# Optimization experiments

Hardware: AMD Instinct MI355X
Metric: run time of the kernel (lower is better)

Reference implementation:

```python
import jax, jax.numpy as jnp
import numpy as np

N_NODES = 20000   # N
N_EDGES = 320000  # E (avg degree 16)
T_STEPS = 16      # T
IN_FEATS = 1      # F
HG = 64           # hidden_g
HT = 128          # hidden_t
LN_EPS = 1e-5


def _layer_norm(x, g, b):
    mu = jnp.mean(x, axis=-1, keepdims=True)
    var = jnp.mean((x - mu) ** 2, axis=-1, keepdims=True)
    return (x - mu) * jax.lax.rsqrt(var + LN_EPS) * g + b


def setup_inputs() -> dict:
    key = jax.random.key(0)
    k = jax.random.split(key, 16)
    r = lambda i, shape, s: jax.random.normal(k[i], shape, jnp.float32) * s
    return dict(
        x_seq=jax.random.normal(k[0], (1, T_STEPS, N_NODES, IN_FEATS), jnp.float32),
        edge_index=jax.random.randint(k[1], (2, N_EDGES), 0, N_NODES, dtype=jnp.int32),
        # SAGEConv layer 0: lin_l (aggregated neighbors, has bias) + lin_r (root)
        W_l0=r(2, (IN_FEATS, HG), 0.5), W_r0=r(3, (IN_FEATS, HG), 0.5), b0=jnp.zeros((HG,), jnp.float32),
        ln0_g=jnp.ones((HG,), jnp.float32), ln0_b=jnp.zeros((HG,), jnp.float32),
        # SAGEConv layer 1
        W_l1=r(4, (HG, HG), 0.1), W_r1=r(5, (HG, HG), 0.1), b1=jnp.zeros((HG,), jnp.float32),
        ln1_g=jnp.ones((HG,), jnp.float32), ln1_b=jnp.zeros((HG,), jnp.float32),
        # GRU (torch layout: gates r,z,n stacked along first dim)
        gru_Wih=r(6, (3 * HT, HG), 0.05), gru_Whh=r(7, (3 * HT, HT), 0.05),
        gru_bih=jnp.zeros((3 * HT,), jnp.float32), gru_bhh=jnp.zeros((3 * HT,), jnp.float32),
        # head
        head_W=r(8, (HT, 1), 0.05), head_b=jnp.zeros((1,), jnp.float32),
    )


def reference(x_seq, edge_index, W_l0, W_r0, b0, ln0_g, ln0_b,
              W_l1, W_r1, b1, ln1_g, ln1_b,
              gru_Wih, gru_Whh, gru_bih, gru_bhh, head_W, head_b):
    src, dst = edge_index[0], edge_index[1]
    # in-degree for mean aggregation (clamped to 1, like PyG mean aggr on isolated nodes)
    deg = jnp.clip(jax.ops.segment_sum(jnp.ones((N_EDGES,), jnp.float32), dst,
                                       num_segments=N_NODES), 1.0)[:, None]

    def sage(x, Wl, Wr, b):
        # mean over incoming neighbors, then lin_l(aggr) + lin_r(root)
        agg = jax.ops.segment_sum(x[src], dst, num_segments=N_NODES) / deg
        return agg @ Wl + x @ Wr + b

    def stack(xt):  # xt: (N, F) -> (N, HG); dropout is identity in eval mode
        h = jax.nn.relu(_layer_norm(sage(xt, W_l0, W_r0, b0), ln0_g, ln0_b))
        h = jax.nn.relu(_layer_norm(sage(h, W_l1, W_r1, b1), ln1_g, ln1_b))
        return h

    X = x_seq[0]  # (T, N, F), B == 1
    # scan over timesteps (matches the per-t Python loop, bounds peak memory)
    _, H = jax.lax.scan(lambda c, xt: (c, stack(xt)), None, X)  # H: (T, N, HG)

    def gru_step(h, xt):  # torch GRU cell; batch = N nodes
        gi = xt @ gru_Wih.T + gru_bih
        gh = h @ gru_Whh.T + gru_bhh
        ir, iz, inn = jnp.split(gi, 3, axis=-1)
        hr, hz, hn = jnp.split(gh, 3, axis=-1)
        r = jax.nn.sigmoid(ir + hr)
        z = jax.nn.sigmoid(iz + hz)
        n = jnp.tanh(inn + r * hn)
        return (1.0 - z) * n + z * h, None

    h0 = jnp.zeros((N_NODES, HT), x_seq.dtype)
    hT, _ = jax.lax.scan(gru_step, h0, H)
    y = (hT @ head_W + head_b)[:, 0]  # (N,)
    return y
```

## Files before the change

### kernel.cpp

```cpp
#include <hip/hip_runtime.h>
#include <math.h>

#define NN 20000
#define NE 320000
#define TS 16
#define HG 64
#define HTT 128
#define NG 384
#define LN_EPS 1e-5f

typedef __attribute__((ext_vector_type(8))) _Float16 f16x8;
typedef __attribute__((ext_vector_type(4))) _Float16 f16x4;
typedef __attribute__((ext_vector_type(2))) _Float16 f16x2;
typedef __attribute__((ext_vector_type(4))) float f32x4;

__device__ __forceinline__ float wave_sum64(float v) {
  #pragma unroll
  for (int off = 32; off > 0; off >>= 1) v += __shfl_xor(v, off, 64);
  return v;
}
__device__ __forceinline__ float quad_sum16(float v) {
  #pragma unroll
  for (int off = 1; off < 16; off <<= 1) v += __shfl_xor(v, off, 64);
  return v;
}
__device__ __forceinline__ float fast_sigmoid(float x) {
  return __builtin_amdgcn_rcpf(1.f + __expf(-x));
}
__device__ __forceinline__ float fast_tanh(float x) {
  float e = __expf(-2.f * fabsf(x));
  float th = (1.f - e) * __builtin_amdgcn_rcpf(1.f + e);
  return copysignf(th, x);
}

__global__ __launch_bounds__(256) void k_setup(
    const float* __restrict__ x_seq, float* __restrict__ xT,
    const float* __restrict__ Wih, _Float16* __restrict__ WihF,
    const float* __restrict__ Whh, _Float16* __restrict__ WhhF,
    const float* __restrict__ Wl1, const float* __restrict__ Wr1,
    _Float16* __restrict__ Wchi, _Float16* __restrict__ Wclo,
    const float* __restrict__ Wl0, const float* __restrict__ Wr0,
    const float* __restrict__ b0, const float* __restrict__ g0,
    const float* __restrict__ be0, float* __restrict__ P,
    int* __restrict__ cnt) {
  int gid = blockIdx.x * 256 + threadIdx.x;
  int stride = gridDim.x * 256;
  for (int i = gid; i < NN * TS; i += stride) {
    int t = i / NN, n = i - t * NN;
    xT[n * 16 + t] = x_seq[i];
  }
  for (int i = gid; i < NG * HG; i += stride) WihF[i] = (_Float16)Wih[i];
  for (int i = gid; i < NG * HTT; i += stride) WhhF[i] = (_Float16)Whh[i];
  for (int i = gid; i < HG * 128; i += stride) {
    int n = i >> 7, k = i & 127;
    float x = (k < HG) ? Wl1[k * HG + n] : Wr1[(k - HG) * HG + n];
    _Float16 h = (_Float16)x;
    Wchi[i] = h;
    Wclo[i] = (_Float16)(x - (float)h);
  }
  for (int i = gid; i < NN; i += stride) cnt[i] = 0;
  if (blockIdx.x == 0 && threadIdx.x < 64) {
    int f = threadIdx.x;
    float u = Wl0[f], v = Wr0[f], c = b0[f], g = g0[f];
    float um = wave_sum64(u) * (1.f / 64.f);
    float vm = wave_sum64(v) * (1.f / 64.f);
    float cm = wave_sum64(c) * (1.f / 64.f);
    float uc = u - um, vc = v - vm, cc = c - cm;
    float muu = wave_sum64(uc * uc) * (1.f / 64.f);
    float mvv = wave_sum64(vc * vc) * (1.f / 64.f);
    float mcc = wave_sum64(cc * cc) * (1.f / 64.f);
    float muv = wave_sum64(uc * vc) * (1.f / 64.f);
    float muc = wave_sum64(uc * cc) * (1.f / 64.f);
    float mvc = wave_sum64(vc * cc) * (1.f / 64.f);
    P[f] = uc * g; P[64 + f] = vc * g; P[128 + f] = cc * g; P[192 + f] = be0[f];
    if (f == 0) {
      P[256] = muu; P[257] = mvv; P[258] = mcc;
      P[259] = muv; P[260] = muc; P[261] = mvc;
    }
  }
}

__global__ void k_hist(const int* __restrict__ dst, int* cnt) {
  int e = blockIdx.x * blockDim.x + threadIdx.x;
  if (e < NE) atomicAdd(&cnt[dst[e]], 1);
}

__global__ void k_scan(int* cnt, int* row_ptr, float* deg_inv) {
  __shared__ int s[1024];
  const int PER = 20;
  int tid = threadIdx.x;
  int base = tid * PER;
  int vloc[PER], dloc[PER];
  int sum = 0;
  #pragma unroll
  for (int j = 0; j < PER; j++) {
    int n = base + j;
    int d = (n < NN) ? cnt[n] : 0;
    vloc[j] = sum;
    dloc[j] = d;
    sum += d;
  }
  s[tid] = sum;
  __syncthreads();
  for (int off = 1; off < 1024; off <<= 1) {
    int t = (tid >= off) ? s[tid - off] : 0;
    __syncthreads();
    s[tid] += t;
    __syncthreads();
  }
  int excl = s[tid] - sum;
  #pragma unroll
  for (int j = 0; j < PER; j++) {
    int n = base + j;
    if (n < NN) {
      int rp = excl + vloc[j];
      row_ptr[n] = rp;
      cnt[n] = rp;
      int d = dloc[j];
      deg_inv[n] = 1.0f / (float)((d > 1) ? d : 1);
    }
  }
  if (tid == 1023) row_ptr[NN] = s[1023];
}

__global__ void k_fill(const int* __restrict__ src, const int* __restrict__ dst,
                       int* cursor, int* col) {
  int e = blockIdx.x * blockDim.x + threadIdx.x;
  if (e < NE) {
    int p = atomicAdd(&cursor[dst[e]], 1);
    col[p] = src[e];
  }
}

__global__ __launch_bounds__(256) void k_h0_fused(
    const float* __restrict__ xT,
    const int* __restrict__ row_ptr, const int* __restrict__ col,
    const float* __restrict__ deg_inv,
    const float* __restrict__ P,
    _Float16* __restrict__ h0r,
    _Float16* __restrict__ code2) {
  int lane = threadIdx.x & 63;
  int n = blockIdx.x * 4 + (threadIdx.x >> 6);
  int grp = lane >> 4, tl = lane & 15;
  int beg = row_ptr[n];
  int deg = row_ptr[n + 1] - beg;
  float s0 = 0.f, s1 = 0.f;
  int iters = (deg + 7) >> 3;
  for (int it = 0; it < iters; it++) {
    int e0 = it * 8 + grp, e1 = it * 8 + 4 + grp;
    bool v0 = e0 < deg, v1 = e1 < deg;
    int i0 = v0 ? e0 : 0, i1 = v1 ? e1 : 0;
    int c0 = col[beg + i0];
    int c1 = col[beg + i1];
    float x0 = xT[c0 * 16 + tl];
    float x1 = xT[c1 * 16 + tl];
    s0 += v0 ? x0 : 0.f;
    s1 += v1 ? x1 : 0.f;
  }
  float s = s0 + s1;
  s += __shfl_xor(s, 16, 64);
  s += __shfl_xor(s, 32, 64);
  float aggv = s * deg_inv[n];
  float xv = xT[n * 16 + tl];
  float muu = P[256], mvv = P[257], mcc = P[258];
  float muv = P[259], muc = P[260], mvc = P[261];
  if (lane < 16) {
    float a = aggv, x = xv;
    float var = a * a * muu + x * x * mvv + mcc
              + 2.f * (a * x * muv + a * muc + x * mvc);
    float rstd = rsqrtf(var + LN_EPS);
    _Float16 Ah = (_Float16)(a * rstd);
    _Float16 Xh = (_Float16)(x * rstd);
    _Float16 Ch = (_Float16)rstd;
    f16x8 cw = {Ah, Ah, Xh, Xh, Ch, Ch, (_Float16)0.f, (_Float16)0.f};
    *(f16x8*)&code2[(size_t)n * 128 + (lane & 7) * 16 + (lane >> 3) * 8] = cw;
  }
  #pragma unroll
  for (int half = 0; half < 2; half++) {
    int c = lane + half * 64;
    int t = c >> 3, f8 = (c & 7) * 8;
    float a = __shfl(aggv, t, 64);
    float x = __shfl(xv, t, 64);
    float var = a * a * muu + x * x * mvv + mcc
              + 2.f * (a * x * muv + a * muc + x * mvc);
    float rstd = rsqrtf(var + LN_EPS);
    f16x8 o;
    #pragma unroll
    for (int j = 0; j < 8; j++) {
      int f = f8 + j;
      float d = a * P[f] + x * P[64 + f] + P[128 + f];
      o[j] = (_Float16)fmaxf(d * rstd + P[192 + f], 0.f);
    }
    *(f16x8*)&h0r[(size_t)n * 1024 + c * 8] = o;
  }
}

__global__ __launch_bounds__(256) void k_gather(
    const int* __restrict__ row_ptr, const int* __restrict__ col,
    const _Float16* __restrict__ code2,
    const float* __restrict__ P,
    _Float16* __restrict__ agg) {
  int lane = threadIdx.x & 63;
  int n = blockIdx.x * 4 + (threadIdx.x >> 6);
  const f16x2 h2z = {(_Float16)0.f, (_Float16)0.f};
  const f16x2 h2o = {(_Float16)1.f, (_Float16)1.f};
  int f1 = (lane & 7) * 8;
  int tmod = lane >> 3;
  f16x2 Pu2[4], Pv2[4], Pc2[4], Pb2[4];
  #pragma unroll
  for (int j = 0; j < 4; j++) {
    Pu2[j] = (f16x2){(_Float16)P[f1 + 2*j],       (_Float16)P[f1 + 2*j + 1]};
    Pv2[j] = (f16x2){(_Float16)P[64 + f1 + 2*j],  (_Float16)P[64 + f1 + 2*j + 1]};
    Pc2[j] = (f16x2){(_Float16)P[128 + f1 + 2*j], (_Float16)P[128 + f1 + 2*j + 1]};
    Pb2[j] = (f16x2){(_Float16)P[192 + f1 + 2*j], (_Float16)P[192 + f1 + 2*j + 1]};
  }
  int beg = row_ptr[n];
  int deg = row_ptr[n + 1] - beg;
  int cvAll = (lane < deg) ? col[beg + lane] : 0;

  f16x2 aE1[4], aO1[4], aE2[4], aO2[4];
  #pragma unroll
  for (int j = 0; j < 4; j++) { aE1[j] = h2z; aO1[j] = h2z; aE2[j] = h2z; aO2[j] = h2z; }

#define ACC_SET(c, mk, FULL, ACC)                                          \
  { f16x2 _A = __builtin_shufflevector(c, c, 0, 1);                        \
    f16x2 _X = __builtin_shufflevector(c, c, 2, 3);                        \
    f16x2 _C = __builtin_shufflevector(c, c, 4, 5);                        \
    _Pragma("unroll")                                                      \
    for (int j = 0; j < 4; j++) {                                          \
      f16x2 d = __builtin_elementwise_fma(_A, Pu2[j],                      \
                 __builtin_elementwise_fma(_X, Pv2[j],                     \
                  __builtin_elementwise_fma(_C, Pc2[j], Pb2[j])));         \
      d = __builtin_elementwise_max(d, h2z);                               \
      ACC[j] = (FULL) ? (ACC[j] + d)                                       \
                      : __builtin_elementwise_fma(d, mk, ACC[j]);          \
    } }

#define LOADBLK(CA, CB, EB)                                                \
  { _Pragma("unroll")                                                      \
    for (int e = 0; e < 4; e++) {                                          \
      int c = __builtin_amdgcn_readlane(cvAll, (EB) + e);                  \
      const _Float16* cp = code2 + (size_t)c * 128 + tmod * 16;            \
      CA[e] = *(const f16x8*)cp;                                           \
      CB[e] = *(const f16x8*)(cp + 8);                                     \
    } }

#define ACCBLK(CA, CB, EB)                                                 \
  { if ((EB) + 4 <= deg) {                                                 \
      _Pragma("unroll")                                                    \
      for (int e = 0; e < 4; e++) {                                        \
        if (e & 1) { ACC_SET(CA[e], h2o, true, aO1) ACC_SET(CB[e], h2o, true, aO2) } \
        else       { ACC_SET(CA[e], h2o, true, aE1) ACC_SET(CB[e], h2o, true, aE2) } \
      }                                                                    \
    } else {                                                               \
      _Pragma("unroll")                                                    \
      for (int e = 0; e < 4; e++) {                                        \
        f16x2 mk = (((EB) + e) < deg) ? h2o : h2z;                         \
        if (e & 1) { ACC_SET(CA[e], mk, false, aO1) ACC_SET(CB[e], mk, false, aO2) } \
        else       { ACC_SET(CA[e], mk, false, aE1) ACC_SET(CB[e], mk, false, aE2) } \
      }                                                                    \
    } }

  int nb4 = (deg + 3) >> 2;
  if (nb4 > 16) nb4 = 16;
  {
    f16x8 cA[4], cB[4], nA[4], nB[4];
    if (nb4 > 0) LOADBLK(cA, cB, 0)
    int b = 0;
    while (b < nb4) {
      if (b + 1 < nb4) LOADBLK(nA, nB, (b + 1) << 2)
      ACCBLK(cA, cB, b << 2)
      b++;
      if (b >= nb4) break;
      if (b + 1 < nb4) LOADBLK(cA, cB, (b + 1) << 2)
      ACCBLK(nA, nB, b << 2)
      b++;
    }
  }
  for (int e = 64; e < deg; e++) {
    int c = col[beg + e];
    const _Float16* cp = code2 + (size_t)c * 128 + tmod * 16;
    f16x8 ca = *(const f16x8*)cp;
    f16x8 cb = *(const f16x8*)(cp + 8);
    ACC_SET(ca, h2o, true, aE1) ACC_SET(cb, h2o, true, aE2)
  }
#undef ACCBLK
#undef LOADBLK
#undef ACC_SET

  float dif = 1.0f / (float)((deg > 1) ? deg : 1);
  _Float16 dih = (_Float16)dif;
  f16x2 di2 = {dih, dih};
  union { f16x8 v; f16x2 h[4]; } u0, u1;
  #pragma unroll
  for (int j = 0; j < 4; j++) {
    u0.h[j] = (aE1[j] + aO1[j]) * di2;
    u1.h[j] = (aE2[j] + aO2[j]) * di2;
  }
  *(f16x8*)&agg[(size_t)n * 1024 + lane * 8] = u0.v;
  *(f16x8*)&agg[(size_t)n * 1024 + 512 + lane * 8] = u1.v;
}

__global__ __launch_bounds__(256) void k_gemm(
    const _Float16* __restrict__ h0r,
    const _Float16* __restrict__ agg,
    const _Float16* __restrict__ Wchi, const _Float16* __restrict__ Wclo,
    const float* __restrict__ b1, const float* __restrict__ g1, const float* __restrict__ be1,
    _Float16* __restrict__ Ht_all) {
  int tid = threadIdx.x;
  int lane = tid & 63, wave = tid >> 6;
  int col16 = lane & 15, quad = lane >> 4;
  int m0 = blockIdx.x * 16;

  float bias[4], gg[4], bb[4];
  #pragma unroll
  for (int nt = 0; nt < 4; nt++) {
    int nf = nt * 16 + col16;
    bias[nt] = b1[nf]; gg[nt] = g1[nf]; bb[nt] = be1[nf];
  }
  size_t rowbase = (size_t)(m0 + col16) * 1024;

  for (int ts = 0; ts < 4; ts++) {
    int t = wave * 4 + ts;
    f32x4 acc[4];
    #pragma unroll
    for (int nt = 0; nt < 4; nt++) acc[nt] = (f32x4){0.f, 0.f, 0.f, 0.f};

    f16x8 aa[2], ar[2];
    #pragma unroll
    for (int kk = 0; kk < 2; kk++) {
      aa[kk] = *(const f16x8*)&agg[rowbase + t * 64 + kk * 32 + quad * 8];
      ar[kk] = *(const f16x8*)&h0r[rowbase + t * 64 + kk * 32 + quad * 8];
    }
    #pragma unroll
    for (int kk = 0; kk < 2; kk++) {
      #pragma unroll
      for (int nt = 0; nt < 4; nt++) {
        int nf = nt * 16 + col16;
        f16x8 bh = *(const f16x8*)&Wchi[nf * 128 + kk * 32 + quad * 8];
        f16x8 bl = *(const f16x8*)&Wclo[nf * 128 + kk * 32 + quad * 8];
        acc[nt] = __builtin_amdgcn_mfma_f32_16x16x32_f16(aa[kk], bh, acc[nt], 0, 0, 0);
        acc[nt] = __builtin_amdgcn_mfma_f32_16x16x32_f16(aa[kk], bl, acc[nt], 0, 0, 0);
      }
    }
    #pragma unroll
    for (int kk = 0; kk < 2; kk++) {
      #pragma unroll
      for (int nt = 0; nt < 4; nt++) {
        int nf = nt * 16 + col16;
        f16x8 bh = *(const f16x8*)&Wchi[nf * 128 + 64 + kk * 32 + quad * 8];
        f16x8 bl = *(const f16x8*)&Wclo[nf * 128 + 64 + kk * 32 + quad * 8];
        acc[nt] = __builtin_amdgcn_mfma_f32_16x16x32_f16(ar[kk], bh, acc[nt], 0, 0, 0);
        acc[nt] = __builtin_amdgcn_mfma_f32_16x16x32_f16(ar[kk], bl, acc[nt], 0, 0, 0);
      }
    }

    #pragma unroll
    for (int r = 0; r < 4; r++) {
      float v[4];
      #pragma unroll
      for (int nt = 0; nt < 4; nt++) v[nt] = acc[nt][r] + bias[nt];
      float s = (v[0] + v[1]) + (v[2] + v[3]);
      float mu = quad_sum16(s) * (1.f / 64.f);
      float sq = 0.f;
      #pragma unroll
      for (int nt = 0; nt < 4; nt++) { v[nt] -= mu; sq += v[nt] * v[nt]; }
      float var = quad_sum16(sq) * (1.f / 64.f);
      float rstd = rsqrtf(var + LN_EPS);
      int m = m0 + quad * 4 + r;
      size_t base = ((size_t)t * NN + m) * HG;
      #pragma unroll
      for (int nt = 0; nt < 4; nt++) {
        float o = fmaxf(v[nt] * rstd * gg[nt] + bb[nt], 0.f);
        Ht_all[base + nt * 16 + col16] = (_Float16)o;
      }
    }
  }
}

__global__ __launch_bounds__(256, 2) void k_gru_all(
    const _Float16* __restrict__ Ht_all,
    const _Float16* __restrict__ WihF,
    const _Float16* __restrict__ WhhF,
    const float* __restrict__ bih, const float* __restrict__ bhh,
    const float* __restrict__ headW, const float* __restrict__ headb,
    float* __restrict__ out) {
  __shared__ _Float16 WihL[NG * 64];
  __shared__ _Float16 hL[2][32 * 128];
  __shared__ float yL[4][32];

  int tid = threadIdx.x;
  int lane = tid & 63, wave = tid >> 6;
  int col16 = lane & 15, quad = lane >> 4;
  int m0 = blockIdx.x * 32;
  int gb = 2 * wave;

  for (int i = tid; i < NG * 8; i += 256) {
    int g = i >> 3, k8 = i & 7;
    *(f16x8*)&WihL[g * 64 + ((k8 + g) & 7) * 8] = *(const f16x8*)&WihF[g * 64 + k8 * 8];
  }
  for (int i = tid; i < 2 * 32 * 128; i += 256) hL[0][i] = (_Float16)0.f;

  int gts[6];
  #pragma unroll
  for (int t6 = 0; t6 < 6; t6++)
    gts[t6] = (t6 < 2) ? (gb + t6) : (t6 < 4) ? (8 + gb + t6 - 2) : (16 + gb + t6 - 4);

  f16x8 wgh[4][6];
  #pragma unroll
  for (int kk = 0; kk < 4; kk++)
    #pragma unroll
    for (int t6 = 0; t6 < 6; t6++)
      wgh[kk][t6] = *(const f16x8*)&WhhF[(size_t)(gts[t6] * 16 + col16) * HTT + kk * 32 + quad * 8];

  float bR[2], bZ[2], bNi[2], bNh[2], hw[2];
  int waddr[2][4][2];
  #pragma unroll
  for (int js = 0; js < 2; js++) {
    int j = (gb + js) * 16 + col16;
    bR[js]  = bih[j] + bhh[j];
    bZ[js]  = bih[HTT + j] + bhh[HTT + j];
    bNi[js] = bih[2 * HTT + j];
    bNh[js] = bhh[2 * HTT + j];
    hw[js]  = headW[j];
    #pragma unroll
    for (int mt = 0; mt < 2; mt++)
      #pragma unroll
      for (int r = 0; r < 4; r++) {
        int row = mt * 16 + quad * 4 + r;
        waddr[mt][r][js] = row * 128 + (((j >> 3) + row) & 15) * 8 + (j & 7);
      }
  }
  float hreg[2][4][2];
  #pragma unroll
  for (int mt = 0; mt < 2; mt++)
    #pragma unroll
    for (int r = 0; r < 4; r++) { hreg[mt][r][0] = 0.f; hreg[mt][r][1] = 0.f; }

  size_t aoff[2][2];
  #pragma unroll
  for (int kk = 0; kk < 2; kk++)
    #pragma unroll
    for (int mt = 0; mt < 2; mt++)
      aoff[kk][mt] = (size_t)(m0 + mt * 16 + col16) * HG + kk * 32 + quad * 8;

  f16x8 gah[2][2];
  #pragma unroll
  for (int kk = 0; kk < 2; kk++)
    #pragma unroll
    for (int mt = 0; mt < 2; mt++)
      gah[kk][mt] = *(const f16x8*)&Ht_all[aoff[kk][mt]];

  __syncthreads();

  for (int t = 0; t < TS; t++) {
    const _Float16* hcur = hL[t & 1];
    _Float16* hnxt = hL[(t + 1) & 1];

    f32x4 acc[8][2];
    #pragma unroll
    for (int a = 0; a < 8; a++) {
      acc[a][0] = (f32x4){0.f, 0.f, 0.f, 0.f};
      acc[a][1] = (f32x4){0.f, 0.f, 0.f, 0.f};
    }

    #pragma unroll
    for (int kk = 0; kk < 2; kk++) {
      #pragma unroll
      for (int t6 = 0; t6 < 6; t6++) {
        int g = gts[t6] * 16 + col16;
        int k8 = kk * 4 + quad;
        f16x8 b = *(const f16x8*)&WihL[g * 64 + ((k8 + g) & 7) * 8];
        #pragma unroll
        for (int mt = 0; mt < 2; mt++)
          acc[t6][mt] = __builtin_amdgcn_mfma_f32_16x16x32_f16(gah[kk][mt], b, acc[t6][mt], 0, 0, 0);
      }
    }

    if (t + 1 < TS) {
      const _Float16* AHn = Ht_all + (size_t)(t + 1) * NN * HG;
      #pragma unroll
      for (int kk = 0; kk < 2; kk++)
        #pragma unroll
        for (int mt = 0; mt < 2; mt++)
          gah[kk][mt] = *(const f16x8*)&AHn[aoff[kk][mt]];
    }

    #pragma unroll
    for (int kk = 0; kk < 4; kk++) {
      f16x8 ah[2];
      #pragma unroll
      for (int mt = 0; mt < 2; mt++) {
        int row = mt * 16 + col16;
        int k8 = kk * 4 + quad;
        ah[mt] = *(const f16x8*)&hcur[row * 128 + ((k8 + row) & 15) * 8];
      }
      #pragma unroll
      for (int t6 = 0; t6 < 6; t6++) {
        int ai = (t6 < 4) ? t6 : t6 + 2;
        #pragma unroll
        for (int mt = 0; mt < 2; mt++)
          acc[ai][mt] = __builtin_amdgcn_mfma_f32_16x16x32_f16(ah[mt], wgh[kk][t6], acc[ai][mt], 0, 0, 0);
      }
    }

    #pragma unroll
    for (int mt = 0; mt < 2; mt++) {
      #pragma unroll
      for (int r = 0; r < 4; r++) {
        #pragma unroll
        for (int js = 0; js < 2; js++) {
          float R  = acc[0 + js][mt][r] + bR[js];
          float Z  = acc[2 + js][mt][r] + bZ[js];
          float Ni = acc[4 + js][mt][r] + bNi[js];
          float Nh = acc[6 + js][mt][r] + bNh[js];
          float rg = fast_sigmoid(R);
          float zg = fast_sigmoid(Z);
          float nn = fast_tanh(Ni + rg * Nh);
          float hn = nn + zg * (hreg[mt][r][js] - nn);
          hreg[mt][r][js] = hn;
          hnxt[waddr[mt][r][js]] = (_Float16)hn;
        }
      }
    }
    __syncthreads();
  }

  #pragma unroll
  for (int mt = 0; mt < 2; mt++) {
    #pragma unroll
    for (int r = 0; r < 4; r++) {
      float py = hreg[mt][r][0] * hw[0] + hreg[mt][r][1] * hw[1];
      py = quad_sum16(py);
      if (col16 == 0) yL[wave][mt * 16 + quad * 4 + r] = py;
    }
  }
  __syncthreads();
  if (tid < 32)
    out[m0 + tid] = yL[0][tid] + yL[1][tid] + yL[2][tid] + yL[3][tid] + headb[0];
}

extern "C" void kernel_launch(void* const* d_in, const int* in_sizes, int n_in,
                              void* d_out, int out_size, void* d_ws, size_t ws_size,
                              hipStream_t stream) {
  const float* x_seq = (const float*)d_in[0];
  const int*   edge  = (const int*)d_in[1];
  const float* Wl0   = (const float*)d_in[2];
  const float* Wr0   = (const float*)d_in[3];
  const float* b0    = (const float*)d_in[4];
  const float* g0    = (const float*)d_in[5];
  const float* be0   = (const float*)d_in[6];
  const float* Wl1   = (const float*)d_in[7];
  const float* Wr1   = (const float*)d_in[8];
  const float* b1    = (const float*)d_in[9];
  const float* g1    = (const float*)d_in[10];
  const float* be1   = (const float*)d_in[11];
  const float* Wih   = (const float*)d_in[12];
  const float* Whh   = (const float*)d_in[13];
  const float* bih   = (const float*)d_in[14];
  const float* bhh   = (const float*)d_in[15];
  const float* headW = (const float*)d_in[16];
  const float* headb = (const float*)d_in[17];
  float* out = (float*)d_out;

  const int* srcp = edge;
  const int* dstp = edge + NE;

  char* ws = (char*)d_ws;
  size_t off = 0;
  auto alloc = [&](size_t bytes) -> void* {
    void* p = ws + off;
    off += (bytes + 255) & ~(size_t)255;
    return p;
  };
  int*   cnt     = (int*)alloc(NN * 4);
  int*   row_ptr = (int*)alloc((NN + 1) * 4);
  int*   col     = (int*)alloc(NE * 4);
  float* deg_inv = (float*)alloc(NN * 4);
  float* xT      = (float*)alloc((size_t)NN * TS * 4);
  float* P       = (float*)alloc(512 * 4);
  _Float16* h0r  = (_Float16*)alloc((size_t)NN * 1024 * 2);
  _Float16* code2= (_Float16*)alloc((size_t)NN * 128 * 2);
  _Float16* agg  = (_Float16*)alloc((size_t)NN * 1024 * 2);
  _Float16* Ht_all = (_Float16*)alloc((size_t)TS * NN * HG * 2);
  _Float16* WihF = (_Float16*)alloc((size_t)NG * HG * 2);
  _Float16* WhhF = (_Float16*)alloc((size_t)NG * HTT * 2);
  _Float16* Wchi = (_Float16*)alloc((size_t)HG * 128 * 2);
  _Float16* Wclo = (_Float16*)alloc((size_t)HG * 128 * 2);
  (void)ws_size; (void)in_sizes; (void)n_in; (void)out_size;

  k_setup<<<1250, 256, 0, stream>>>(x_seq, xT, Wih, WihF, Whh, WhhF,
                                    Wl1, Wr1, Wchi, Wclo,
                                    Wl0, Wr0, b0, g0, be0, P, cnt);
  k_hist<<<(NE + 255) / 256, 256, 0, stream>>>(dstp, cnt);
  k_scan<<<1, 1024, 0, stream>>>(cnt, row_ptr, deg_inv);
  k_fill<<<(NE + 255) / 256, 256, 0, stream>>>(srcp, dstp, cnt, col);
  k_h0_fused<<<NN / 4, 256, 0, stream>>>(xT, row_ptr, col, deg_inv, P, h0r, code2);
  k_gather<<<NN / 4, 256, 0, stream>>>(row_ptr, col, code2, P, agg);
  k_gemm<<<NN / 16, 256, 0, stream>>>(h0r, agg, Wchi, Wclo, b1, g1, be1, Ht_all);
  k_gru_all<<<NN / 32, 256, 0, stream>>>(Ht_all, WihF, WhhF, bih, bhh,
                                         headW, headb, out);
}
```

Baseline: 384.6 us.

## Recompute layer-0 activations in GEMM from compact code; fold histogram into setup

Stops materializing the full layer-0 activation tensor h0r (N×16×64 fp16). The GEMM kernel now rebuilds each root row from the per-node, per-timestep code (a·rstd, x·rstd, rstd) and the precomputed LN parameters using packed fp16 FMAs. This removes a large global write and read. The edge in-degree histogram also moves into the setup kernel, and a memset zeroes the counts, which drops one launch. The cost is extra ALU work in the GEMM, and the affine and ReLU now run in fp16 instead of fp32, which may add rounding error.

```diff
diff --git a/kernel.cpp b/kernel.cpp
--- a/kernel.cpp
+++ b/kernel.cpp
@@ -42,13 +42,14 @@
     const float* __restrict__ Wl0, const float* __restrict__ Wr0,
     const float* __restrict__ b0, const float* __restrict__ g0,
     const float* __restrict__ be0, float* __restrict__ P,
-    int* __restrict__ cnt) {
+    const int* __restrict__ dst, int* __restrict__ cnt) {
   int gid = blockIdx.x * 256 + threadIdx.x;
   int stride = gridDim.x * 256;
   for (int i = gid; i < NN * TS; i += stride) {
     int t = i / NN, n = i - t * NN;
     xT[n * 16 + t] = x_seq[i];
   }
+  for (int i = gid; i < NE; i += stride) atomicAdd(&cnt[dst[i]], 1);
   for (int i = gid; i < NG * HG; i += stride) WihF[i] = (_Float16)Wih[i];
   for (int i = gid; i < NG * HTT; i += stride) WhhF[i] = (_Float16)Whh[i];
   for (int i = gid; i < HG * 128; i += stride) {
@@ -58,7 +59,6 @@
     Wchi[i] = h;
     Wclo[i] = (_Float16)(x - (float)h);
   }
-  for (int i = gid; i < NN; i += stride) cnt[i] = 0;
   if (blockIdx.x == 0 && threadIdx.x < 64) {
     int f = threadIdx.x;
     float u = Wl0[f], v = Wr0[f], c = b0[f], g = g0[f];
@@ -80,11 +80,6 @@
   }
 }
 
-__global__ void k_hist(const int* __restrict__ dst, int* cnt) {
-  int e = blockIdx.x * blockDim.x + threadIdx.x;
-  if (e < NE) atomicAdd(&cnt[dst[e]], 1);
-}
-
 __global__ void k_scan(int* cnt, int* row_ptr, float* deg_inv) {
   __shared__ int s[1024];
   const int PER = 20;
@@ -132,12 +127,11 @@
   }
 }
 
-__global__ __launch_bounds__(256) void k_h0_fused(
+__global__ __launch_bounds__(256) void k_code(
     const float* __restrict__ xT,
     const int* __restrict__ row_ptr, const int* __restrict__ col,
     const float* __restrict__ deg_inv,
     const float* __restrict__ P,
-    _Float16* __restrict__ h0r,
     _Float16* __restrict__ code2) {
   int lane = threadIdx.x & 63;
   int n = blockIdx.x * 4 + (threadIdx.x >> 6);
@@ -162,9 +156,9 @@
   s += __shfl_xor(s, 32, 64);
   float aggv = s * deg_inv[n];
   float xv = xT[n * 16 + tl];
-  float muu = P[256], mvv = P[257], mcc = P[258];
-  float muv = P[259], muc = P[260], mvc = P[261];
   if (lane < 16) {
+    float muu = P[256], mvv = P[257], mcc = P[258];
+    float muv = P[259], muc = P[260], mvc = P[261];
     float a = aggv, x = xv;
     float var = a * a * muu + x * x * mvv + mcc
               + 2.f * (a * x * muv + a * muc + x * mvc);
@@ -174,24 +168,6 @@
     _Float16 Ch = (_Float16)rstd;
     f16x8 cw = {Ah, Ah, Xh, Xh, Ch, Ch, (_Float16)0.f, (_Float16)0.f};
     *(f16x8*)&code2[(size_t)n * 128 + (lane & 7) * 16 + (lane >> 3) * 8] = cw;
-  }
-  #pragma unroll
-  for (int half = 0; half < 2; half++) {
-    int c = lane + half * 64;
-    int t = c >> 3, f8 = (c & 7) * 8;
-    float a = __shfl(aggv, t, 64);
-    float x = __shfl(xv, t, 64);
-    float var = a * a * muu + x * x * mvv + mcc
-              + 2.f * (a * x * muv + a * muc + x * mvc);
-    float rstd = rsqrtf(var + LN_EPS);
-    f16x8 o;
-    #pragma unroll
-    for (int j = 0; j < 8; j++) {
-      int f = f8 + j;
-      float d = a * P[f] + x * P[64 + f] + P[128 + f];
-      o[j] = (_Float16)fmaxf(d * rstd + P[192 + f], 0.f);
-    }
-    *(f16x8*)&h0r[(size_t)n * 1024 + c * 8] = o;
   }
 }
 
@@ -302,7 +278,9 @@
 }
 
 __global__ __launch_bounds__(256) void k_gemm(
-    const _Float16* __restrict__ h0r,
+    const int* __restrict__ row_ptr,
+    const _Float16* __restrict__ code2,
+    const float* __restrict__ P,
     const _Float16* __restrict__ agg,
     const _Float16* __restrict__ Wchi, const _Float16* __restrict__ Wclo,
     const float* __restrict__ b1, const float* __restrict__ g1, const float* __restrict__ be1,
@@ -311,6 +289,7 @@
   int lane = tid & 63, wave = tid >> 6;
   int col16 = lane & 15, quad = lane >> 4;
   int m0 = blockIdx.x * 16;
+  (void)row_ptr;
 
   float bias[4], gg[4], bb[4];
   #pragma unroll
@@ -318,6 +297,19 @@
     int nf = nt * 16 + col16;
     bias[nt] = b1[nf]; gg[nt] = g1[nf]; bb[nt] = be1[nf];
   }
+  const f16x2 h2z = {(_Float16)0.f, (_Float16)0.f};
+  f16x2 Pu2[2][4], Pv2[2][4], Pc2[2][4], Pb2[2][4];
+  #pragma unroll
+  for (int kk = 0; kk < 2; kk++)
+    #pragma unroll
+    for (int jj = 0; jj < 4; jj++) {
+      int f = kk * 32 + quad * 8 + jj * 2;
+      Pu2[kk][jj] = (f16x2){(_Float16)P[f],       (_Float16)P[f + 1]};
+      Pv2[kk][jj] = (f16x2){(_Float16)P[64 + f],  (_Float16)P[64 + f + 1]};
+      Pc2[kk][jj] = (f16x2){(_Float16)P[128 + f], (_Float16)P[128 + f + 1]};
+      Pb2[kk][jj] = (f16x2){(_Float16)P[192 + f], (_Float16)P[192 + f + 1]};
+    }
+  const _Float16* myc = code2 + (size_t)(m0 + col16) * 128;
   size_t rowbase = (size_t)(m0 + col16) * 1024;
 
   for (int ts = 0; ts < 4; ts++) {
@@ -326,12 +318,26 @@
     #pragma unroll
     for (int nt = 0; nt < 4; nt++) acc[nt] = (f32x4){0.f, 0.f, 0.f, 0.f};
 
-    f16x8 aa[2], ar[2];
-    #pragma unroll
-    for (int kk = 0; kk < 2; kk++) {
+    f16x8 aa[2];
+    #pragma unroll
+    for (int kk = 0; kk < 2; kk++)
       aa[kk] = *(const f16x8*)&agg[rowbase + t * 64 + kk * 32 + quad * 8];
-      ar[kk] = *(const f16x8*)&h0r[rowbase + t * 64 + kk * 32 + quad * 8];
-    }
+
+    f16x8 cw = *(const f16x8*)&myc[(t & 7) * 16 + (t >> 3) * 8];
+    f16x2 cA = __builtin_shufflevector(cw, cw, 0, 1);
+    f16x2 cX = __builtin_shufflevector(cw, cw, 2, 3);
+    f16x2 cC = __builtin_shufflevector(cw, cw, 4, 5);
+    union { f16x8 v; f16x2 h[4]; } ur[2];
+    #pragma unroll
+    for (int kk = 0; kk < 2; kk++)
+      #pragma unroll
+      for (int jj = 0; jj < 4; jj++) {
+        f16x2 d = __builtin_elementwise_fma(cA, Pu2[kk][jj],
+                   __builtin_elementwise_fma(cX, Pv2[kk][jj],
+                    __builtin_elementwise_fma(cC, Pc2[kk][jj], Pb2[kk][jj])));
+        ur[kk].h[jj] = __builtin_elementwise_max(d, h2z);
+      }
+
     #pragma unroll
     for (int kk = 0; kk < 2; kk++) {
       #pragma unroll
@@ -350,8 +356,8 @@
         int nf = nt * 16 + col16;
         f16x8 bh = *(const f16x8*)&Wchi[nf * 128 + 64 + kk * 32 + quad * 8];
         f16x8 bl = *(const f16x8*)&Wclo[nf * 128 + 64 + kk * 32 + quad * 8];
-        acc[nt] = __builtin_amdgcn_mfma_f32_16x16x32_f16(ar[kk], bh, acc[nt], 0, 0, 0);
-        acc[nt] = __builtin_amdgcn_mfma_f32_16x16x32_f16(ar[kk], bl, acc[nt], 0, 0, 0);
+        acc[nt] = __builtin_amdgcn_mfma_f32_16x16x32_f16(ur[kk].v, bh, acc[nt], 0, 0, 0);
+        acc[nt] = __builtin_amdgcn_mfma_f32_16x16x32_f16(ur[kk].v, bl, acc[nt], 0, 0, 0);
       }
     }
 
@@ -579,7 +585,6 @@
   float* deg_inv = (float*)alloc(NN * 4);
   float* xT      = (float*)alloc((size_t)NN * TS * 4);
   float* P       = (float*)alloc(512 * 4);
-  _Float16* h0r  = (_Float16*)alloc((size_t)NN * 1024 * 2);
   _Float16* code2= (_Float16*)alloc((size_t)NN * 128 * 2);
   _Float16* agg  = (_Float16*)alloc((size_t)NN * 1024 * 2);
   _Float16* Ht_all = (_Float16*)alloc((size_t)TS * NN * HG * 2);
@@ -589,15 +594,16 @@
   _Float16* Wclo = (_Float16*)alloc((size_t)HG * 128 * 2);
   (void)ws_size; (void)in_sizes; (void)n_in; (void)out_size;
 
+  hipMemsetAsync(cnt, 0, NN * 4, stream);
   k_setup<<<1250, 256, 0, stream>>>(x_seq, xT, Wih, WihF, Whh, WhhF,
                                     Wl1, Wr1, Wchi, Wclo,
-                                    Wl0, Wr0, b0, g0, be0, P, cnt);
-  k_hist<<<(NE + 255) / 256, 256, 0, stream>>>(dstp, cnt);
+                                    Wl0, Wr0, b0, g0, be0, P, dstp, cnt);
   k_scan<<<1, 1024, 0, stream>>>(cnt, row_ptr, deg_inv);
   k_fill<<<(NE + 255) / 256, 256, 0, stream>>>(srcp, dstp, cnt, col);
-  k_h0_fused<<<NN / 4, 256, 0, stream>>>(xT, row_ptr, col, deg_inv, P, h0r, code2);
+  k_code<<<NN / 4, 256, 0, stream>>>(xT, row_ptr, col, deg_inv, P, code2);
   k_gather<<<NN / 4, 256, 0, stream>>>(row_ptr, col, code2, P, agg);
-  k_gemm<<<NN / 16, 256, 0, stream>>>(h0r, agg, Wchi, Wclo, b1, g1, be1, Ht_all);
+  k_gemm<<<NN / 16, 256, 0, stream>>>(row_ptr, code2, P, agg, Wchi, Wclo,
+                                      b1, g1, be1, Ht_all);
   k_gru_all<<<NN / 32, 256, 0, stream>>>(Ht_all, WihF, WhhF, bih, bhh,
                                          headW, headb, out);
 }
```

Measured after the change: 416.1 us. 8.2% more time.
